# Kernel optimization log

Hardware: AMD Instinct MI355X
Metric: run time of the kernel (lower is better)

The kernel has to match this reference:

```python
import jax, jax.numpy as jnp
import numpy as np

N = 50000
E = 800000
D_IN = 128
D_HID = 128
D_OUT = 64
BN_EPS = 1e-5


def setup_inputs() -> dict:
    key = jax.random.key(0)
    ks = jax.random.split(key, 16)
    s = lambda k, shp, fan: jax.random.normal(k, shp, dtype=jnp.float32) / np.sqrt(fan)
    return {
        "x": jax.random.normal(ks[0], (N, D_IN), dtype=jnp.float32),
        "edge_index": jax.random.randint(ks[1], (2, E), 0, N, dtype=jnp.int64),
        # layer 1: SAGEConv(in -> hid)
        "w1l": s(ks[2], (D_IN, D_HID), D_IN),
        "w1r": s(ks[3], (D_IN, D_HID), D_IN),
        "b1": jnp.zeros((D_HID,), jnp.float32),
        "g1": jnp.ones((D_HID,), jnp.float32),
        "be1": jnp.zeros((D_HID,), jnp.float32),
        # layer 2: SAGEConv(hid -> hid)
        "w2l": s(ks[4], (D_HID, D_HID), D_HID),
        "w2r": s(ks[5], (D_HID, D_HID), D_HID),
        "b2": jnp.zeros((D_HID,), jnp.float32),
        "g2": jnp.ones((D_HID,), jnp.float32),
        "be2": jnp.zeros((D_HID,), jnp.float32),
        # layer 3: SAGEConv(hid -> out)
        "w3l": s(ks[6], (D_HID, D_OUT), D_HID),
        "w3r": s(ks[7], (D_HID, D_OUT), D_HID),
        "b3": jnp.zeros((D_OUT,), jnp.float32),
    }


def sage_conv(x, src, dst, wl, wr, b):
    # mean aggregation of source-node features onto destination nodes
    msg_sum = jax.ops.segment_sum(x[src], dst, num_segments=N)  # [N, d]
    deg = jax.ops.segment_sum(jnp.ones((src.shape[0],), x.dtype), dst, num_segments=N)
    mean = msg_sum / jnp.maximum(deg, 1.0)[:, None]
    return mean @ wl + x @ wr + b


def batch_norm(x, g, b):
    mu = jnp.mean(x, axis=0)
    var = jnp.var(x, axis=0)
    return (x - mu) * jax.lax.rsqrt(var + BN_EPS) * g + b


def reference(x, edge_index, w1l, w1r, b1, g1, be1, w2l, w2r, b2, g2, be2, w3l, w3r, b3):
    src, dst = edge_index[0], edge_index[1]
    h = sage_conv(x, src, dst, w1l, w1r, b1)
    h = jax.nn.relu(batch_norm(h, g1, be1))
    h = sage_conv(h, src, dst, w2l, w2r, b2)
    h = jax.nn.relu(batch_norm(h, g2, be2))
    return sage_conv(h, src, dst, w3l, w3r, b3)
```

## Files before the change

### kernel.cpp

```cpp
#include <hip/hip_runtime.h>
#include <hip/hip_bf16.h>

#define NN 50000
#define NE 800000
#define DH 128
#define NB1 196
#define NBK 391
#define EPB 2048
#define CAPB 4096

typedef __attribute__((ext_vector_type(8))) short bf16x8;
typedef __attribute__((ext_vector_type(4))) float f32x4;
typedef __attribute__((ext_vector_type(8))) unsigned short us8;
typedef __attribute__((ext_vector_type(4))) unsigned short us4;

__device__ __forceinline__ unsigned short f2bf(float f) {
  unsigned int u = __builtin_bit_cast(unsigned int, f);
  unsigned int r = (u + 0x7FFFu + ((u >> 16) & 1u)) >> 16;
  return (unsigned short)r;
}
__device__ __forceinline__ float bf2f(unsigned int h16) {
  unsigned int u = h16 << 16;
  return __builtin_bit_cast(float, u);
}

__global__ __launch_bounds__(256) void k_prep(const float* __restrict__ x,
                                              const float* __restrict__ w1l, const float* __restrict__ w1r,
                                              const float* __restrict__ w2l, const float* __restrict__ w2r,
                                              const float* __restrict__ w3l, const float* __restrict__ w3r,
                                              unsigned short* __restrict__ xb,
                                              unsigned short* __restrict__ w1t,
                                              unsigned short* __restrict__ w2t,
                                              unsigned short* __restrict__ w3t) {
  int b = blockIdx.x, t = threadIdx.x;
  if (b < 3125) {
    int i = b * 256 + t;
    const float4* p = reinterpret_cast<const float4*>(x) + (size_t)i * 2;
    float4 a = p[0], bb = p[1];
    us8 o;
    o[0] = f2bf(a.x); o[1] = f2bf(a.y); o[2] = f2bf(a.z); o[3] = f2bf(a.w);
    o[4] = f2bf(bb.x); o[5] = f2bf(bb.y); o[6] = f2bf(bb.z); o[7] = f2bf(bb.w);
    reinterpret_cast<us8*>(xb)[i] = o;
  } else if (b < 3381) {
    bool is1 = b < 3253;
    int idx = (b - (is1 ? 3125 : 3253)) * 256 + t;
    int c = idx >> 8, k = idx & 255;
    const float* wl = is1 ? w1l : w2l;
    const float* wr = is1 ? w1r : w2r;
    float v = (k < DH) ? wl[k * DH + c] : wr[(k - DH) * DH + c];
    (is1 ? w1t : w2t)[idx] = f2bf(v);
  } else {
    int idx = (b - 3381) * 256 + t;
    int c = idx >> 7, k = idx & 127;
    float v = (c < 64) ? w3l[k * 64 + c] : w3r[k * 64 + (c - 64)];
    w3t[idx] = f2bf(v);
  }
}

__global__ __launch_bounds__(256) void k_bucket(const int* __restrict__ src,
                                                const int* __restrict__ dst,
                                                int* __restrict__ bcnt,
                                                int* __restrict__ ebuf) {
  __shared__ int lcnt[NBK], lbase[NBK];
  int t = threadIdx.x;
  for (int b = t; b < NBK; b += 256) lcnt[b] = 0;
  __syncthreads();
  int base = blockIdx.x * EPB;
  int d[8], s[8];
#pragma unroll
  for (int i = 0; i < 8; ++i) {
    int e = base + i * 256 + t;
    if (e < NE) { d[i] = dst[e]; s[i] = src[e]; }
    else d[i] = -1;
  }
#pragma unroll
  for (int i = 0; i < 8; ++i)
    if (d[i] >= 0) atomicAdd(&lcnt[d[i] >> 7], 1);
  __syncthreads();
  for (int b = t; b < NBK; b += 256) {
    int c = lcnt[b];
    lbase[b] = c > 0 ? atomicAdd(&bcnt[b], c) : 0;
    lcnt[b] = 0;
  }
  __syncthreads();
#pragma unroll
  for (int i = 0; i < 8; ++i) {
    if (d[i] >= 0) {
      int b = d[i] >> 7;
      int r = atomicAdd(&lcnt[b], 1);
      ebuf[(size_t)b * CAPB + lbase[b] + r] = s[i] | ((d[i] & 127) << 20);
    }
  }
}

__global__ __launch_bounds__(256) void k_hist(const int* __restrict__ bcnt,
                                              const int* __restrict__ ebuf,
                                              int* __restrict__ deg,
                                              float* __restrict__ invd) {
  int b = blockIdx.x;
  __shared__ int h[128];
  int t = threadIdx.x;
  if (t < 128) h[t] = 0;
  __syncthreads();
  int cnt = bcnt[b];
  const int* eb = ebuf + (size_t)b * CAPB;
  for (int e = t; e < cnt; e += 256)
    atomicAdd(&h[(eb[e] >> 20) & 127], 1);
  __syncthreads();
  int i = (b << 7) + t;
  if (t < 128 && i < NN) {
    int d = h[t];
    deg[i] = d;
    invd[i] = 1.0f / (float)(d > 0 ? d : 1);
  }
}

__global__ void k_scan1(const int* __restrict__ deg, int* __restrict__ iscan,
                        int* __restrict__ bsum) {
  __shared__ int s[256];
  int t = threadIdx.x;
  int i = blockIdx.x * 256 + t;
  int d = (i < NN) ? deg[i] : 0;
  s[t] = d;
  __syncthreads();
  for (int off = 1; off < 256; off <<= 1) {
    int v = (t >= off) ? s[t - off] : 0;
    __syncthreads();
    s[t] += v;
    __syncthreads();
  }
  if (i < NN) iscan[i] = s[t];
  if (t == 255) bsum[blockIdx.x] = s[255];
}

__global__ void k_scan2(int* __restrict__ bsum) {
  __shared__ int s[256];
  int t = threadIdx.x;
  int v = (t < NB1) ? bsum[t] : 0;
  s[t] = v;
  __syncthreads();
  for (int off = 1; off < 256; off <<= 1) {
    int u = (t >= off) ? s[t - off] : 0;
    __syncthreads();
    s[t] += u;
    __syncthreads();
  }
  if (t < NB1) bsum[t] = s[t] - v;
}

__global__ void k_scan3(const int* __restrict__ deg, const int* __restrict__ iscan,
                        const int* __restrict__ bsum, int* __restrict__ rowptr) {
  int i = blockIdx.x * 256 + threadIdx.x;
  if (i >= NN) return;
  int excl = bsum[blockIdx.x] + iscan[i] - deg[i];
  rowptr[i] = excl;
  if (i == 0) rowptr[NN] = NE;
}

__global__ __launch_bounds__(256) void k_fill2(const int* __restrict__ rowptr,
                                               const int* __restrict__ bcnt,
                                               const int* __restrict__ ebuf,
                                               int* __restrict__ adj) {
  int b = blockIdx.x;
  int n0 = b << 7;
  int n1 = n0 + 128; if (n1 > NN) n1 = NN;
  __shared__ int cur[128];
  int t = threadIdx.x;
  if (t < n1 - n0) cur[t] = rowptr[n0 + t];
  __syncthreads();
  int cnt = bcnt[b];
  const int* eb = ebuf + (size_t)b * CAPB;
  for (int e = t; e < cnt; e += 256) {
    int p = eb[e];
    int pos = atomicAdd(&cur[(p >> 20) & 127], 1);
    adj[pos] = p & 0xFFFFF;
  }
}

template <bool BNA>
__global__ __launch_bounds__(256) void k_agg(const unsigned short* __restrict__ h,
                                             const int* __restrict__ rowptr,
                                             const int* __restrict__ adj,
                                             const float* __restrict__ invd,
                                             const float* __restrict__ stats,
                                             const float* __restrict__ g,
                                             const float* __restrict__ be,
                                             unsigned short* __restrict__ meanb) {
  int wid = (blockIdx.x * blockDim.x + threadIdx.x) >> 6;
  int lane = threadIdx.x & 63;
  if (wid >= NN) return;
  int lo = rowptr[wid], hi = rowptr[wid + 1];
  int q = lane >> 4;
  int c = (lane & 15) << 3;
  float sc[8], sh[8];
  if (BNA) {
#pragma unroll
    for (int j = 0; j < 8; ++j) {
      int col = c + j;
      float mu = stats[col] * (1.0f / NN);
      float var = stats[128 + col] * (1.0f / NN) - mu * mu;
      float rs = rsqrtf(var + 1e-5f);
      sc[j] = rs * g[col];
      sh[j] = be[col] - mu * sc[j];
    }
  }
  float a[8] = {};
  int e = lo;
#pragma unroll 2
  for (; e + 4 <= hi; e += 4) {
    int s = adj[e + q];
    us8 v = *reinterpret_cast<const us8*>(h + (size_t)s * DH + c);
#pragma unroll
    for (int j = 0; j < 8; ++j) {
      float f = bf2f(v[j]);
      a[j] += BNA ? fmaxf(f * sc[j] + sh[j], 0.0f) : f;
    }
  }
  if (q < hi - e) {
    int s = adj[e + q];
    us8 v = *reinterpret_cast<const us8*>(h + (size_t)s * DH + c);
#pragma unroll
    for (int j = 0; j < 8; ++j) {
      float f = bf2f(v[j]);
      a[j] += BNA ? fmaxf(f * sc[j] + sh[j], 0.0f) : f;
    }
  }
#pragma unroll
  for (int j = 0; j < 8; ++j) {
    a[j] += __shfl_xor(a[j], 16);
    a[j] += __shfl_xor(a[j], 32);
  }
  if (q == 0) {
    float iv = invd[wid];
    us8 o;
#pragma unroll
    for (int j = 0; j < 8; ++j) o[j] = f2bf(a[j] * iv);
    *reinterpret_cast<us8*>(meanb + (size_t)wid * DH + c) = o;
  }
}

__global__ __launch_bounds__(256) void k_agg3(const unsigned short* __restrict__ t3,
                                              const int* __restrict__ rowptr,
                                              const int* __restrict__ adj,
                                              const float* __restrict__ invd,
                                              const float* __restrict__ b3,
                                              float* __restrict__ out) {
  int wid = (blockIdx.x * blockDim.x + threadIdx.x) >> 6;
  int lane = threadIdx.x & 63;
  if (wid >= NN) return;
  int lo = rowptr[wid], hi = rowptr[wid + 1];
  int q = lane >> 4;
  int c = (lane & 15) << 2;
  float a[4] = {};
  int e = lo;
#pragma unroll 2
  for (; e + 4 <= hi; e += 4) {
    int s = adj[e + q];
    us4 v = *reinterpret_cast<const us4*>(t3 + (size_t)s * 128 + c);
#pragma unroll
    for (int j = 0; j < 4; ++j) a[j] += bf2f(v[j]);
  }
  if (q < hi - e) {
    int s = adj[e + q];
    us4 v = *reinterpret_cast<const us4*>(t3 + (size_t)s * 128 + c);
#pragma unroll
    for (int j = 0; j < 4; ++j) a[j] += bf2f(v[j]);
  }
#pragma unroll
  for (int j = 0; j < 4; ++j) {
    a[j] += __shfl_xor(a[j], 16);
    a[j] += __shfl_xor(a[j], 32);
  }
  if (q == 0) {
    float iv = invd[wid];
    us4 w = *reinterpret_cast<const us4*>(t3 + (size_t)wid * 128 + 64 + c);
    float4 o;
    o.x = a[0] * iv + bf2f(w[0]) + b3[c + 0];
    o.y = a[1] * iv + bf2f(w[1]) + b3[c + 1];
    o.z = a[2] * iv + bf2f(w[2]) + b3[c + 2];
    o.w = a[3] * iv + bf2f(w[3]) + b3[c + 3];
    *reinterpret_cast<float4*>(out + (size_t)wid * 64 + c) = o;
  }
}

template <bool SPLIT, bool STATS, bool APPLY>
__global__ __launch_bounds__(256) void k_gemm(const unsigned short* __restrict__ Am,
                                              const unsigned short* __restrict__ Ah,
                                              const unsigned short* __restrict__ Wt,
                                              const float* __restrict__ bias,
                                              const float* __restrict__ stA,
                                              const float* __restrict__ gA,
                                              const float* __restrict__ beA,
                                              unsigned short* __restrict__ outb,
                                              float* __restrict__ stats) {
  constexpr int KS = SPLIT ? 8 : 4;
  constexpr int WK = KS * 32;
  __shared__ float asc[DH], ash[DH];
  if (APPLY) {
    int t = threadIdx.x;
    if (t < DH) {
      float mu = stA[t] * (1.0f / NN);
      float var = stA[128 + t] * (1.0f / NN) - mu * mu;
      float rs = rsqrtf(var + 1e-5f);
      float scv = rs * gA[t];
      asc[t] = scv;
      ash[t] = beA[t] - mu * scv;
    }
    __syncthreads();
  }
  int lane = threadIdx.x & 63;
  int w = threadIdx.x >> 6;
  int wr = w >> 1, wc = w & 1;
  int rowbase = blockIdx.x * 128 + wr * 64;
  int colbase = wc * 64;
  int lr = lane & 15, lk = (lane >> 4) << 3;

  f32x4 acc[4][4] = {};
#pragma unroll
  for (int ks = 0; ks < KS; ++ks) {
    const unsigned short* Ab = (!SPLIT || ks < 4) ? Am : Ah;
    bool tr = APPLY && (!SPLIT || ks >= 4);
    int ka = ((ks & 3) << 5) + lk;
    int kw = (ks << 5) + lk;
    bf16x8 af[4], bfr[4];
#pragma unroll
    for (int i = 0; i < 4; ++i) {
      int r = rowbase + i * 16 + lr;
      r = r < NN ? r : NN - 1;
      us8 raw = *reinterpret_cast<const us8*>(Ab + (size_t)r * DH + ka);
      if (tr) {
        us8 o;
#pragma unroll
        for (int j = 0; j < 8; ++j) {
          float f = bf2f(raw[j]);
          o[j] = f2bf(fmaxf(f * asc[ka + j] + ash[ka + j], 0.0f));
        }
        af[i] = __builtin_bit_cast(bf16x8, o);
      } else {
        af[i] = __builtin_bit_cast(bf16x8, raw);
      }
    }
#pragma unroll
    for (int j = 0; j < 4; ++j)
      bfr[j] = *reinterpret_cast<const bf16x8*>(Wt + (size_t)(colbase + j * 16 + lr) * WK + kw);
#pragma unroll
    for (int i = 0; i < 4; ++i)
#pragma unroll
      for (int j = 0; j < 4; ++j)
        acc[i][j] = __builtin_amdgcn_mfma_f32_16x16x32_bf16(af[i], bfr[j], acc[i][j], 0, 0, 0);
  }

  float bv[4];
#pragma unroll
  for (int j = 0; j < 4; ++j) bv[j] = bias ? bias[colbase + j * 16 + lr] : 0.0f;

  float s1[4] = {}, s2[4] = {};
#pragma unroll
  for (int i = 0; i < 4; ++i) {
#pragma unroll
    for (int j = 0; j < 4; ++j) {
      int col = colbase + j * 16 + lr;
#pragma unroll
      for (int r = 0; r < 4; ++r) {
        int row = rowbase + i * 16 + ((lane >> 4) << 2) + r;
        if (row < NN) {
          float val = acc[i][j][r] + bv[j];
          outb[(size_t)row * 128 + col] = f2bf(val);
          if (STATS) { s1[j] += val; s2[j] += val * val; }
        }
      }
    }
  }

  if (STATS) {
    __shared__ float sd[2][128][2];
#pragma unroll
    for (int j = 0; j < 4; ++j) {
      s1[j] += __shfl_xor(s1[j], 16);
      s1[j] += __shfl_xor(s1[j], 32);
      s2[j] += __shfl_xor(s2[j], 16);
      s2[j] += __shfl_xor(s2[j], 32);
    }
    if (lane < 16) {
#pragma unroll
      for (int j = 0; j < 4; ++j) {
        sd[wr][colbase + j * 16 + lane][0] = s1[j];
        sd[wr][colbase + j * 16 + lane][1] = s2[j];
      }
    }
    __syncthreads();
    int t = threadIdx.x;
    if (t < 128) {
      atomicAdd(&stats[t], sd[0][t][0] + sd[1][t][0]);
      atomicAdd(&stats[128 + t], sd[0][t][1] + sd[1][t][1]);
    }
  }
}

extern "C" void kernel_launch(void* const* d_in, const int* in_sizes, int n_in,
                              void* d_out, int out_size, void* d_ws, size_t ws_size,
                              hipStream_t stream) {
  const float* x = (const float*)d_in[0];
  const int* ei = (const int*)d_in[1];
  const int* srcp = ei;
  const int* dstp = ei + NE;
  const float* w1l = (const float*)d_in[2];
  const float* w1r = (const float*)d_in[3];
  const float* b1 = (const float*)d_in[4];
  const float* g1 = (const float*)d_in[5];
  const float* be1 = (const float*)d_in[6];
  const float* w2l = (const float*)d_in[7];
  const float* w2r = (const float*)d_in[8];
  const float* b2 = (const float*)d_in[9];
  const float* g2 = (const float*)d_in[10];
  const float* be2 = (const float*)d_in[11];
  const float* w3l = (const float*)d_in[12];
  const float* w3r = (const float*)d_in[13];
  const float* b3 = (const float*)d_in[14];

  char* ws = (char*)d_ws;
  size_t off = 0;
  auto alloc = [&](size_t bytes) {
    char* p = ws + off;
    off = (off + bytes + 255) & ~(size_t)255;
    return p;
  };
  unsigned short* xb = (unsigned short*)alloc((size_t)NN * DH * 2);
  unsigned short* meanb = (unsigned short*)alloc((size_t)NN * DH * 2);
  unsigned short* gbuf1 = (unsigned short*)alloc((size_t)NN * DH * 2);
  unsigned short* gbuf2 = (unsigned short*)alloc((size_t)NN * DH * 2);
  unsigned short* w1t = (unsigned short*)alloc(128 * 256 * 2);
  unsigned short* w2t = (unsigned short*)alloc(128 * 256 * 2);
  unsigned short* w3t = (unsigned short*)alloc(128 * 128 * 2);
  int* bcnt = (int*)alloc(NBK * 4);
  float* stats1 = (float*)alloc(2 * DH * 4);
  float* stats2 = (float*)alloc(2 * DH * 4);
  size_t zlen = (char*)(stats2 + 2 * DH) - (char*)bcnt;
  int* deg = (int*)alloc(NN * 4);
  int* rowptr = (int*)alloc((NN + 1) * 4);
  int* adj = (int*)alloc((size_t)NE * 4);
  int* ebuf = (int*)alloc((size_t)NBK * CAPB * 4);
  float* invd = (float*)alloc(NN * 4);
  int* iscan = (int*)alloc(NN * 4);
  int* bsum = (int*)alloc(NB1 * 4);

  hipMemsetAsync(bcnt, 0, zlen, stream);
  k_prep<<<3445, 256, 0, stream>>>(x, w1l, w1r, w2l, w2r, w3l, w3r, xb, w1t, w2t, w3t);
  k_bucket<<<(NE + EPB - 1) / EPB, 256, 0, stream>>>(srcp, dstp, bcnt, ebuf);
  k_hist<<<NBK, 256, 0, stream>>>(bcnt, ebuf, deg, invd);
  k_scan1<<<NB1, 256, 0, stream>>>(deg, iscan, bsum);
  k_scan2<<<1, 256, 0, stream>>>(bsum);
  k_scan3<<<NB1, 256, 0, stream>>>(deg, iscan, bsum, rowptr);
  k_fill2<<<NBK, 256, 0, stream>>>(rowptr, bcnt, ebuf, adj);

  int agg_blocks = (NN * 64 + 255) / 256;
  int gemm_blocks = (NN + 127) / 128;

  k_agg<false><<<agg_blocks, 256, 0, stream>>>(xb, rowptr, adj, invd, nullptr, nullptr, nullptr, meanb);
  k_gemm<true, true, false><<<gemm_blocks, 256, 0, stream>>>(
      meanb, xb, w1t, b1, nullptr, nullptr, nullptr, gbuf1, stats1);

  k_agg<true><<<agg_blocks, 256, 0, stream>>>(gbuf1, rowptr, adj, invd, stats1, g1, be1, meanb);
  k_gemm<true, true, true><<<gemm_blocks, 256, 0, stream>>>(
      meanb, gbuf1, w2t, b2, stats1, g1, be1, gbuf2, stats2);

  k_gemm<false, false, true><<<gemm_blocks, 256, 0, stream>>>(
      gbuf2, nullptr, w3t, nullptr, stats2, g2, be2, gbuf1, nullptr);
  k_agg3<<<agg_blocks, 256, 0, stream>>>(gbuf1, rowptr, adj, invd, b3, (float*)d_out);
}
```

Before: 221.8 us.

## Materialize BN+ReLU once in a separate pass and unroll gather loops deeper

Batch-norm plus ReLU is no longer applied on the fly inside the aggregation gather and the GEMM A-operand loads. A new elementwise kernel now writes the normalized activations once after each stats GEMM, so the aggregation and GEMM kernels read plain bf16. The aggregation loops in k_agg and k_agg3 are also unrolled to keep four neighbor-row loads in flight per iteration. This removes redundant per-edge normalization arithmetic, but adds two extra launches and a full read/write pass over the N×128 buffer per layer.

```diff
diff --git a/kernel.cpp b/kernel.cpp
--- a/kernel.cpp
+++ b/kernel.cpp
@@ -177,14 +177,10 @@
   }
 }
 
-template <bool BNA>
 __global__ __launch_bounds__(256) void k_agg(const unsigned short* __restrict__ h,
                                              const int* __restrict__ rowptr,
                                              const int* __restrict__ adj,
                                              const float* __restrict__ invd,
-                                             const float* __restrict__ stats,
-                                             const float* __restrict__ g,
-                                             const float* __restrict__ be,
                                              unsigned short* __restrict__ meanb) {
   int wid = (blockIdx.x * blockDim.x + threadIdx.x) >> 6;
   int lane = threadIdx.x & 63;
@@ -192,38 +188,45 @@
   int lo = rowptr[wid], hi = rowptr[wid + 1];
   int q = lane >> 4;
   int c = (lane & 15) << 3;
-  float sc[8], sh[8];
-  if (BNA) {
-#pragma unroll
-    for (int j = 0; j < 8; ++j) {
-      int col = c + j;
-      float mu = stats[col] * (1.0f / NN);
-      float var = stats[128 + col] * (1.0f / NN) - mu * mu;
-      float rs = rsqrtf(var + 1e-5f);
-      sc[j] = rs * g[col];
-      sh[j] = be[col] - mu * sc[j];
-    }
-  }
   float a[8] = {};
   int e = lo;
-#pragma unroll 2
-  for (; e + 4 <= hi; e += 4) {
-    int s = adj[e + q];
-    us8 v = *reinterpret_cast<const us8*>(h + (size_t)s * DH + c);
-#pragma unroll
-    for (int j = 0; j < 8; ++j) {
-      float f = bf2f(v[j]);
-      a[j] += BNA ? fmaxf(f * sc[j] + sh[j], 0.0f) : f;
-    }
+  for (; e + 16 <= hi; e += 16) {
+    int s0 = adj[e + q], s1 = adj[e + 4 + q], s2 = adj[e + 8 + q], s3 = adj[e + 12 + q];
+    us8 v0 = *reinterpret_cast<const us8*>(h + (size_t)s0 * DH + c);
+    us8 v1 = *reinterpret_cast<const us8*>(h + (size_t)s1 * DH + c);
+    us8 v2 = *reinterpret_cast<const us8*>(h + (size_t)s2 * DH + c);
+    us8 v3 = *reinterpret_cast<const us8*>(h + (size_t)s3 * DH + c);
+#pragma unroll
+    for (int j = 0; j < 8; ++j) a[j] += bf2f(v0[j]);
+#pragma unroll
+    for (int j = 0; j < 8; ++j) a[j] += bf2f(v1[j]);
+#pragma unroll
+    for (int j = 0; j < 8; ++j) a[j] += bf2f(v2[j]);
+#pragma unroll
+    for (int j = 0; j < 8; ++j) a[j] += bf2f(v3[j]);
+  }
+  if (e + 8 <= hi) {
+    int s0 = adj[e + q], s1 = adj[e + 4 + q];
+    us8 v0 = *reinterpret_cast<const us8*>(h + (size_t)s0 * DH + c);
+    us8 v1 = *reinterpret_cast<const us8*>(h + (size_t)s1 * DH + c);
+#pragma unroll
+    for (int j = 0; j < 8; ++j) a[j] += bf2f(v0[j]);
+#pragma unroll
+    for (int j = 0; j < 8; ++j) a[j] += bf2f(v1[j]);
+    e += 8;
+  }
+  if (e + 4 <= hi) {
+    int s0 = adj[e + q];
+    us8 v0 = *reinterpret_cast<const us8*>(h + (size_t)s0 * DH + c);
+#pragma unroll
+    for (int j = 0; j < 8; ++j) a[j] += bf2f(v0[j]);
+    e += 4;
   }
   if (q < hi - e) {
-    int s = adj[e + q];
-    us8 v = *reinterpret_cast<const us8*>(h + (size_t)s * DH + c);
-#pragma unroll
-    for (int j = 0; j < 8; ++j) {
-      float f = bf2f(v[j]);
-      a[j] += BNA ? fmaxf(f * sc[j] + sh[j], 0.0f) : f;
-    }
+    int s0 = adj[e + q];
+    us8 v0 = *reinterpret_cast<const us8*>(h + (size_t)s0 * DH + c);
+#pragma unroll
+    for (int j = 0; j < 8; ++j) a[j] += bf2f(v0[j]);
   }
 #pragma unroll
   for (int j = 0; j < 8; ++j) {
@@ -253,18 +256,35 @@
   int c = (lane & 15) << 2;
   float a[4] = {};
   int e = lo;
-#pragma unroll 2
-  for (; e + 4 <= hi; e += 4) {
-    int s = adj[e + q];
-    us4 v = *reinterpret_cast<const us4*>(t3 + (size_t)s * 128 + c);
-#pragma unroll
-    for (int j = 0; j < 4; ++j) a[j] += bf2f(v[j]);
+  for (; e + 16 <= hi; e += 16) {
+    int s0 = adj[e + q], s1 = adj[e + 4 + q], s2 = adj[e + 8 + q], s3 = adj[e + 12 + q];
+    us4 v0 = *reinterpret_cast<const us4*>(t3 + (size_t)s0 * 128 + c);
+    us4 v1 = *reinterpret_cast<const us4*>(t3 + (size_t)s1 * 128 + c);
+    us4 v2 = *reinterpret_cast<const us4*>(t3 + (size_t)s2 * 128 + c);
+    us4 v3 = *reinterpret_cast<const us4*>(t3 + (size_t)s3 * 128 + c);
+#pragma unroll
+    for (int j = 0; j < 4; ++j) a[j] += bf2f(v0[j]) + bf2f(v1[j]) + bf2f(v2[j]) + bf2f(v3[j]);
+  }
+  if (e + 8 <= hi) {
+    int s0 = adj[e + q], s1 = adj[e + 4 + q];
+    us4 v0 = *reinterpret_cast<const us4*>(t3 + (size_t)s0 * 128 + c);
+    us4 v1 = *reinterpret_cast<const us4*>(t3 + (size_t)s1 * 128 + c);
+#pragma unroll
+    for (int j = 0; j < 4; ++j) a[j] += bf2f(v0[j]) + bf2f(v1[j]);
+    e += 8;
+  }
+  if (e + 4 <= hi) {
+    int s0 = adj[e + q];
+    us4 v0 = *reinterpret_cast<const us4*>(t3 + (size_t)s0 * 128 + c);
+#pragma unroll
+    for (int j = 0; j < 4; ++j) a[j] += bf2f(v0[j]);
+    e += 4;
   }
   if (q < hi - e) {
-    int s = adj[e + q];
-    us4 v = *reinterpret_cast<const us4*>(t3 + (size_t)s * 128 + c);
-#pragma unroll
-    for (int j = 0; j < 4; ++j) a[j] += bf2f(v[j]);
+    int s0 = adj[e + q];
+    us4 v0 = *reinterpret_cast<const us4*>(t3 + (size_t)s0 * 128 + c);
+#pragma unroll
+    for (int j = 0; j < 4; ++j) a[j] += bf2f(v0[j]);
   }
 #pragma unroll
   for (int j = 0; j < 4; ++j) {
@@ -283,31 +303,15 @@
   }
 }
 
-template <bool SPLIT, bool STATS, bool APPLY>
+template <bool SPLIT, bool STATS>
 __global__ __launch_bounds__(256) void k_gemm(const unsigned short* __restrict__ Am,
                                               const unsigned short* __restrict__ Ah,
                                               const unsigned short* __restrict__ Wt,
                                               const float* __restrict__ bias,
-                                              const float* __restrict__ stA,
-                                              const float* __restrict__ gA,
-                                              const float* __restrict__ beA,
                                               unsigned short* __restrict__ outb,
                                               float* __restrict__ stats) {
   constexpr int KS = SPLIT ? 8 : 4;
   constexpr int WK = KS * 32;
-  __shared__ float asc[DH], ash[DH];
-  if (APPLY) {
-    int t = threadIdx.x;
-    if (t < DH) {
-      float mu = stA[t] * (1.0f / NN);
-      float var = stA[128 + t] * (1.0f / NN) - mu * mu;
-      float rs = rsqrtf(var + 1e-5f);
-      float scv = rs * gA[t];
-      asc[t] = scv;
-      ash[t] = beA[t] - mu * scv;
-    }
-    __syncthreads();
-  }
   int lane = threadIdx.x & 63;
   int w = threadIdx.x >> 6;
   int wr = w >> 1, wc = w & 1;
@@ -319,7 +323,6 @@
 #pragma unroll
   for (int ks = 0; ks < KS; ++ks) {
     const unsigned short* Ab = (!SPLIT || ks < 4) ? Am : Ah;
-    bool tr = APPLY && (!SPLIT || ks >= 4);
     int ka = ((ks & 3) << 5) + lk;
     int kw = (ks << 5) + lk;
     bf16x8 af[4], bfr[4];
@@ -327,18 +330,7 @@
     for (int i = 0; i < 4; ++i) {
       int r = rowbase + i * 16 + lr;
       r = r < NN ? r : NN - 1;
-      us8 raw = *reinterpret_cast<const us8*>(Ab + (size_t)r * DH + ka);
-      if (tr) {
-        us8 o;
-#pragma unroll
-        for (int j = 0; j < 8; ++j) {
-          float f = bf2f(raw[j]);
-          o[j] = f2bf(fmaxf(f * asc[ka + j] + ash[ka + j], 0.0f));
-        }
-        af[i] = __builtin_bit_cast(bf16x8, o);
-      } else {
-        af[i] = __builtin_bit_cast(bf16x8, raw);
-      }
+      af[i] = *reinterpret_cast<const bf16x8*>(Ab + (size_t)r * DH + ka);
     }
 #pragma unroll
     for (int j = 0; j < 4; ++j)
@@ -395,6 +387,33 @@
       atomicAdd(&stats[128 + t], sd[0][t][1] + sd[1][t][1]);
     }
   }
+}
+
+__global__ __launch_bounds__(256) void k_bnapply(const unsigned short* __restrict__ gin,
+                                                 const float* __restrict__ stats,
+                                                 const float* __restrict__ g,
+                                                 const float* __restrict__ be,
+                                                 unsigned short* __restrict__ hb) {
+  __shared__ float sc[128], sh[128];
+  int t = threadIdx.x;
+  if (t < 128) {
+    float mu = stats[t] * (1.0f / NN);
+    float var = stats[128 + t] * (1.0f / NN) - mu * mu;
+    float rs = rsqrtf(var + 1e-5f);
+    float scv = rs * g[t];
+    sc[t] = scv;
+    sh[t] = be[t] - mu * scv;
+  }
+  __syncthreads();
+  int i = blockIdx.x * 256 + t;
+  if (i >= NN * DH / 8) return;
+  int c = (t * 8) & 127;
+  us8 v = reinterpret_cast<const us8*>(gin)[i];
+  us8 o;
+#pragma unroll
+  for (int j = 0; j < 8; ++j)
+    o[j] = f2bf(fmaxf(bf2f(v[j]) * sc[c + j] + sh[c + j], 0.0f));
+  reinterpret_cast<us8*>(hb)[i] = o;
 }
 
 extern "C" void kernel_launch(void* const* d_in, const int* in_sizes, int n_in,
@@ -427,8 +446,8 @@
   };
   unsigned short* xb = (unsigned short*)alloc((size_t)NN * DH * 2);
   unsigned short* meanb = (unsigned short*)alloc((size_t)NN * DH * 2);
-  unsigned short* gbuf1 = (unsigned short*)alloc((size_t)NN * DH * 2);
-  unsigned short* gbuf2 = (unsigned short*)alloc((size_t)NN * DH * 2);
+  unsigned short* bufA = (unsigned short*)alloc((size_t)NN * DH * 2);
+  unsigned short* bufB = (unsigned short*)alloc((size_t)NN * DH * 2);
   unsigned short* w1t = (unsigned short*)alloc(128 * 256 * 2);
   unsigned short* w2t = (unsigned short*)alloc(128 * 256 * 2);
   unsigned short* w3t = (unsigned short*)alloc(128 * 128 * 2);
@@ -455,16 +474,16 @@
 
   int agg_blocks = (NN * 64 + 255) / 256;
   int gemm_blocks = (NN + 127) / 128;
-
-  k_agg<false><<<agg_blocks, 256, 0, stream>>>(xb, rowptr, adj, invd, nullptr, nullptr, nullptr, meanb);
-  k_gemm<true, true, false><<<gemm_blocks, 256, 0, stream>>>(
-      meanb, xb, w1t, b1, nullptr, nullptr, nullptr, gbuf1, stats1);
-
-  k_agg<true><<<agg_blocks, 256, 0, stream>>>(gbuf1, rowptr, adj, invd, stats1, g1, be1, meanb);
-  k_gemm<true, true, true><<<gemm_blocks, 256, 0, stream>>>(
-      meanb, gbuf1, w2t, b2, stats1, g1, be1, gbuf2, stats2);
-
-  k_gemm<false, false, true><<<gemm_blocks, 256, 0, stream>>>(
-      gbuf2, nullptr, w3t, nullptr, stats2, g2, be2, gbuf1, nullptr);
-  k_agg3<<<agg_blocks, 256, 0, stream>>>(gbuf1, rowptr, adj, invd, b3, (float*)d_out);
-}
+  int bn_blocks = (NN * DH / 8 + 255) / 256;
+
+  k_agg<<<agg_blocks, 256, 0, stream>>>(xb, rowptr, adj, invd, meanb);
+  k_gemm<true, true><<<gemm_blocks, 256, 0, stream>>>(meanb, xb, w1t, b1, bufA, stats1);
+  k_bnapply<<<bn_blocks, 256, 0, stream>>>(bufA, stats1, g1, be1, bufB);
+
+  k_agg<<<agg_blocks, 256, 0, stream>>>(bufB, rowptr, adj, invd, meanb);
+  k_gemm<true, true><<<gemm_blocks, 256, 0, stream>>>(meanb, bufB, w2t, b2, bufA, stats2);
+  k_bnapply<<<bn_blocks, 256, 0, stream>>>(bufA, stats2, g2, be2, bufB);
+
+  k_gemm<false, false><<<gemm_blocks, 256, 0, stream>>>(bufB, nullptr, w3t, nullptr, bufA, nullptr);
+  k_agg3<<<agg_blocks, 256, 0, stream>>>(bufA, rowptr, adj, invd, b3, (float*)d_out);
+}
```

New measurement: 230.6 us. +3.9%, slower.

## Split gather-aggregation into column-slice phases for cache locality, precompute BN affine

Applied to the files above, without the earlier changes.

The gather aggregation kernels are restructured so that each block handles 4 nodes but only a 32-column slice (64 bytes) of the feature row. The grid is divided into phases, one per column slice, and each wave processes 8 edges at a time. The aim is to shrink the working set each phase gathers from so that random neighbor rows stay in L2/MALL cache. The cost is reading adj/rowptr multiple times, plus smaller 8-byte gathers. A small kernel also precomputes the batch-norm scale and shift once instead of every wave recomputing rsqrt.

```diff
diff --git a/kernel.cpp b/kernel.cpp
--- a/kernel.cpp
+++ b/kernel.cpp
@@ -8,6 +8,7 @@
 #define NBK 391
 #define EPB 2048
 #define CAPB 4096
+#define WPB 12500
 
 typedef __attribute__((ext_vector_type(8))) short bf16x8;
 typedef __attribute__((ext_vector_type(4))) float f32x4;
@@ -177,65 +178,73 @@
   }
 }
 
+__global__ void k_bnprep(const float* __restrict__ stats, const float* __restrict__ g,
+                         const float* __restrict__ be, float2* __restrict__ bnt) {
+  int t = threadIdx.x;
+  if (t >= 128) return;
+  float mu = stats[t] * (1.0f / NN);
+  float var = stats[128 + t] * (1.0f / NN) - mu * mu;
+  float rs = rsqrtf(var + 1e-5f);
+  float scv = rs * g[t];
+  bnt[t] = make_float2(scv, be[t] - mu * scv);
+}
+
 template <bool BNA>
 __global__ __launch_bounds__(256) void k_agg(const unsigned short* __restrict__ h,
                                              const int* __restrict__ rowptr,
                                              const int* __restrict__ adj,
                                              const float* __restrict__ invd,
-                                             const float* __restrict__ stats,
-                                             const float* __restrict__ g,
-                                             const float* __restrict__ be,
+                                             const float2* __restrict__ bnt,
                                              unsigned short* __restrict__ meanb) {
-  int wid = (blockIdx.x * blockDim.x + threadIdx.x) >> 6;
+  int bid = blockIdx.x;
+  int ph = bid / WPB;
+  int node = (bid - ph * WPB) * 4 + (threadIdx.x >> 6);
   int lane = threadIdx.x & 63;
-  if (wid >= NN) return;
-  int lo = rowptr[wid], hi = rowptr[wid + 1];
-  int q = lane >> 4;
-  int c = (lane & 15) << 3;
-  float sc[8], sh[8];
+  int q = lane >> 3;
+  int cc = lane & 7;
+  int cbase = ph * 32 + cc * 4;
+  float sc[4], sh[4];
   if (BNA) {
 #pragma unroll
-    for (int j = 0; j < 8; ++j) {
-      int col = c + j;
-      float mu = stats[col] * (1.0f / NN);
-      float var = stats[128 + col] * (1.0f / NN) - mu * mu;
-      float rs = rsqrtf(var + 1e-5f);
-      sc[j] = rs * g[col];
-      sh[j] = be[col] - mu * sc[j];
-    }
-  }
-  float a[8] = {};
+    for (int j = 0; j < 4; ++j) {
+      float2 v = bnt[cbase + j];
+      sc[j] = v.x; sh[j] = v.y;
+    }
+  }
+  int lo = rowptr[node], hi = rowptr[node + 1];
+  const unsigned short* hb = h + cbase;
+  float a[4] = {};
   int e = lo;
-#pragma unroll 2
-  for (; e + 4 <= hi; e += 4) {
+  for (; e + 8 <= hi; e += 8) {
     int s = adj[e + q];
-    us8 v = *reinterpret_cast<const us8*>(h + (size_t)s * DH + c);
-#pragma unroll
-    for (int j = 0; j < 8; ++j) {
+    us4 v = *reinterpret_cast<const us4*>(hb + (size_t)s * DH);
+#pragma unroll
+    for (int j = 0; j < 4; ++j) {
       float f = bf2f(v[j]);
-      a[j] += BNA ? fmaxf(f * sc[j] + sh[j], 0.0f) : f;
+      a[j] += BNA ? fmaxf(fmaf(f, sc[j], sh[j]), 0.0f) : f;
     }
   }
   if (q < hi - e) {
     int s = adj[e + q];
-    us8 v = *reinterpret_cast<const us8*>(h + (size_t)s * DH + c);
-#pragma unroll
-    for (int j = 0; j < 8; ++j) {
+    us4 v = *reinterpret_cast<const us4*>(hb + (size_t)s * DH);
+#pragma unroll
+    for (int j = 0; j < 4; ++j) {
       float f = bf2f(v[j]);
-      a[j] += BNA ? fmaxf(f * sc[j] + sh[j], 0.0f) : f;
-    }
-  }
-#pragma unroll
-  for (int j = 0; j < 8; ++j) {
+      a[j] += BNA ? fmaxf(fmaf(f, sc[j], sh[j]), 0.0f) : f;
+    }
+  }
+#pragma unroll
+  for (int j = 0; j < 4; ++j) {
+    a[j] += __shfl_xor(a[j], 8);
     a[j] += __shfl_xor(a[j], 16);
     a[j] += __shfl_xor(a[j], 32);
   }
-  if (q == 0) {
-    float iv = invd[wid];
-    us8 o;
-#pragma unroll
-    for (int j = 0; j < 8; ++j) o[j] = f2bf(a[j] * iv);
-    *reinterpret_cast<us8*>(meanb + (size_t)wid * DH + c) = o;
+  if (lane < 8) {
+    float iv = invd[node];
+    us4 o;
+#pragma unroll
+    for (int j = 0; j < 4; ++j) o[j] = f2bf(a[j] * iv);
+    *reinterpret_cast<us4*>(meanb + (size_t)node * DH + ph * 32 + lane * 4) = o;
   }
 }
 
@@ -245,41 +254,45 @@
                                               const float* __restrict__ invd,
                                               const float* __restrict__ b3,
                                               float* __restrict__ out) {
-  int wid = (blockIdx.x * blockDim.x + threadIdx.x) >> 6;
+  int bid = blockIdx.x;
+  int ph = bid / WPB;
+  int node = (bid - ph * WPB) * 4 + (threadIdx.x >> 6);
   int lane = threadIdx.x & 63;
-  if (wid >= NN) return;
-  int lo = rowptr[wid], hi = rowptr[wid + 1];
-  int q = lane >> 4;
-  int c = (lane & 15) << 2;
+  int q = lane >> 3;
+  int cc = lane & 7;
+  int cbase = ph * 32 + cc * 4;
+  int lo = rowptr[node], hi = rowptr[node + 1];
+  const unsigned short* tb = t3 + cbase;
   float a[4] = {};
   int e = lo;
-#pragma unroll 2
-  for (; e + 4 <= hi; e += 4) {
+  for (; e + 8 <= hi; e += 8) {
     int s = adj[e + q];
-    us4 v = *reinterpret_cast<const us4*>(t3 + (size_t)s * 128 + c);
+    us4 v = *reinterpret_cast<const us4*>(tb + (size_t)s * 128);
 #pragma unroll
     for (int j = 0; j < 4; ++j) a[j] += bf2f(v[j]);
   }
   if (q < hi - e) {
     int s = adj[e + q];
-    us4 v = *reinterpret_cast<const us4*>(t3 + (size_t)s * 128 + c);
+    us4 v = *reinterpret_cast<const us4*>(tb + (size_t)s * 128);
 #pragma unroll
     for (int j = 0; j < 4; ++j) a[j] += bf2f(v[j]);
   }
 #pragma unroll
   for (int j = 0; j < 4; ++j) {
+    a[j] += __shfl_xor(a[j], 8);
     a[j] += __shfl_xor(a[j], 16);
     a[j] += __shfl_xor(a[j], 32);
   }
-  if (q == 0) {
-    float iv = invd[wid];
-    us4 w = *reinterpret_cast<const us4*>(t3 + (size_t)wid * 128 + 64 + c);
+  if (lane < 8) {
+    float iv = invd[node];
+    int cb = ph * 32 + lane * 4;
+    us4 w = *reinterpret_cast<const us4*>(t3 + (size_t)node * 128 + 64 + cb);
     float4 o;
-    o.x = a[0] * iv + bf2f(w[0]) + b3[c + 0];
-    o.y = a[1] * iv + bf2f(w[1]) + b3[c + 1];
-    o.z = a[2] * iv + bf2f(w[2]) + b3[c + 2];
-    o.w = a[3] * iv + bf2f(w[3]) + b3[c + 3];
-    *reinterpret_cast<float4*>(out + (size_t)wid * 64 + c) = o;
+    o.x = a[0] * iv + bf2f(w[0]) + b3[cb + 0];
+    o.y = a[1] * iv + bf2f(w[1]) + b3[cb + 1];
+    o.z = a[2] * iv + bf2f(w[2]) + b3[cb + 2];
+    o.w = a[3] * iv + bf2f(w[3]) + b3[cb + 3];
+    *reinterpret_cast<float4*>(out + (size_t)node * 64 + cb) = o;
   }
 }
 
@@ -443,6 +456,7 @@
   float* invd = (float*)alloc(NN * 4);
   int* iscan = (int*)alloc(NN * 4);
   int* bsum = (int*)alloc(NB1 * 4);
+  float2* bnt1 = (float2*)alloc(DH * 8);
 
   hipMemsetAsync(bcnt, 0, zlen, stream);
   k_prep<<<3445, 256, 0, stream>>>(x, w1l, w1r, w2l, w2r, w3l, w3r, xb, w1t, w2t, w3t);
@@ -453,18 +467,18 @@
   k_scan3<<<NB1, 256, 0, stream>>>(deg, iscan, bsum, rowptr);
   k_fill2<<<NBK, 256, 0, stream>>>(rowptr, bcnt, ebuf, adj);
 
-  int agg_blocks = (NN * 64 + 255) / 256;
   int gemm_blocks = (NN + 127) / 128;
 
-  k_agg<false><<<agg_blocks, 256, 0, stream>>>(xb, rowptr, adj, invd, nullptr, nullptr, nullptr, meanb);
+  k_agg<false><<<4 * WPB, 256, 0, stream>>>(xb, rowptr, adj, invd, nullptr, meanb);
   k_gemm<true, true, false><<<gemm_blocks, 256, 0, stream>>>(
       meanb, xb, w1t, b1, nullptr, nullptr, nullptr, gbuf1, stats1);
-
-  k_agg<true><<<agg_blocks, 256, 0, stream>>>(gbuf1, rowptr, adj, invd, stats1, g1, be1, meanb);
+  k_bnprep<<<1, 128, 0, stream>>>(stats1, g1, be1, bnt1);
+
+  k_agg<true><<<4 * WPB, 256, 0, stream>>>(gbuf1, rowptr, adj, invd, bnt1, meanb);
   k_gemm<true, true, true><<<gemm_blocks, 256, 0, stream>>>(
       meanb, gbuf1, w2t, b2, stats1, g1, be1, gbuf2, stats2);
 
   k_gemm<false, false, true><<<gemm_blocks, 256, 0, stream>>>(
       gbuf2, nullptr, w3t, nullptr, stats2, g2, be2, gbuf1, nullptr);
-  k_agg3<<<agg_blocks, 256, 0, stream>>>(gbuf1, rowptr, adj, invd, b3, (float*)d_out);
-}
+  k_agg3<<<2 * WPB, 256, 0, stream>>>(gbuf1, rowptr, adj, invd, b3, (float*)d_out);
+}
```

Result: slower. 330.3 us (+48.9%).
